# Optimization experiments

Hardware: AMD Instinct MI355X
Metric: run time of the kernel (lower is better)

Reference implementation:

```python
import jax, jax.numpy as jnp
import numpy as np

B, D = 16384, 512
EPS_COS = 1e-8  # torch cosine_similarity eps


def setup_inputs() -> dict:
    key = jax.random.key(0)
    ks = jax.random.split(key, 8)
    rep1 = jax.random.normal(ks[0], (B, D), jnp.float32)
    rep2 = jax.random.normal(ks[1], (B, D), jnp.float32)
    rep3 = jax.random.normal(ks[2], (B, D), jnp.float32)
    hazard = jax.random.normal(ks[3], (B, 1), jnp.float32)
    # F.nll_loss expects log-probabilities
    score = jax.nn.log_softmax(jax.random.normal(ks[4], (B, 2), jnp.float32), axis=-1)
    time = jax.random.uniform(ks[5], (B,), jnp.float32)
    event = jax.random.randint(ks[6], (B,), 0, 2, dtype=jnp.int32)
    perm = jax.random.permutation(ks[7], B)  # deterministic stand-in for shuffle()
    x1_idx = perm[: B // 2].astype(jnp.int32)
    x2_idx = perm[B // 2 :].astype(jnp.int32)
    return dict(rep1=rep1, rep2=rep2, rep3=rep3, hazard=hazard, score=score,
                time=time, event=event, x1_idx=x1_idx, x2_idx=x2_idx)


def _normalize(r):
    n = jnp.maximum(jnp.linalg.norm(r, axis=-1, keepdims=True), EPS_COS)
    return r / n


def reference(rep1, rep2, rep3, hazard, score, time, event, x1_idx, x2_idx):
    trade_off, margin, alpha, beta = 0.3, 0.2, 0.5, 0.5
    ev_f = event.astype(score.dtype)

    # ---- cross-entropy term: F.nll_loss(log_probs, event) ----
    nll = -jnp.mean(jnp.take_along_axis(score, event[:, None].astype(jnp.int32), axis=1))

    # ---- Cox negative log-likelihood ----
    order = jnp.argsort(-time)            # descending time
    risk = hazard[order, 0]               # [B]
    evs = ev_f[order]
    log_risk = jnp.log(jnp.cumsum(jnp.exp(risk)) + 1e-6)
    cox = -jnp.sum((risk - log_risk) * evs) / (jnp.sum(evs) + 1e-6)

    # ---- contrastive loss (3 modalities, vectorized over pairs) ----
    R = jnp.stack([_normalize(rep1), _normalize(rep2), _normalize(rep3)])  # [M,B,D]
    x = R[:, x1_idx]  # [M,P,D]
    y = R[:, x2_idx]  # [M,P,D]
    pairs = [(0, 1), (0, 2), (1, 2)]
    dis_xx = sum((x[i] * x[j]).sum(-1) for i, j in pairs)  # [P]
    dis_yy = sum((y[i] * y[j]).sum(-1) for i, j in pairs)  # [P]
    dis_xy = (x * y).sum(-1).sum(0)                         # [P]
    con = jnp.mean(jnp.log1p(jnp.exp(margin + dis_xy - alpha * dis_xx - beta * dis_yy)))

    return nll + cox + trade_off * con
```

## Files before the change

### kernel.cpp

```cpp
#include <hip/hip_runtime.h>
#include <math.h>

#define B_N     16384
#define D_N     512
#define NPAIR   8192
#define NBUCKET 16384
#define CON_BLOCKS 2048
#define STAT_BLOCKS 64
#define BIG_BLOCKS (CON_BLOCKS + STAT_BLOCKS)
#define COX_BLOCKS 64

__device__ __forceinline__ float wave_reduce(float v) {
    #pragma unroll
    for (int m = 32; m >= 1; m >>= 1) v += __shfl_xor(v, m, 64);
    return v;
}

__device__ __forceinline__ float dot4(float4 a, float4 b) {
    return a.x*b.x + a.y*b.y + a.z*b.z + a.w*b.w;
}

__device__ __forceinline__ int bucket_of(float t) {
    return min(max((int)(t * 16384.0f), 0), NBUCKET - 1);
}

__device__ __forceinline__ unsigned long long key_of(float t, int i) {
    return (((unsigned long long)__float_as_uint(t)) << 14) |
           (unsigned long long)(B_N - 1 - i);
}

__global__ __launch_bounds__(256) void k_big(
        const float* __restrict__ rep1,
        const float* __restrict__ rep2,
        const float* __restrict__ rep3,
        const float* __restrict__ hazard,
        const float* __restrict__ score,
        const float* __restrict__ time,
        const int*   __restrict__ event,
        const int*   __restrict__ x1_idx,
        const int*   __restrict__ x2_idx,
        float* __restrict__ partCon,
        float* __restrict__ partNll,
        float* __restrict__ partEv,
        float* __restrict__ sumE,
        int*   __restrict__ head,
        int*   __restrict__ next)
{
    __shared__ float sh0[4], sh1[4];
    const int tid  = threadIdx.x;
    const int lane = tid & 63;
    const int wave = tid >> 6;

    if (blockIdx.x < CON_BLOCKS) {
        const int p  = blockIdx.x * 4 + wave;
        const int ia = x1_idx[p];
        const int ib = x2_idx[p];
        const float4* A1 = (const float4*)(rep1 + (size_t)ia * D_N);
        const float4* A2 = (const float4*)(rep2 + (size_t)ia * D_N);
        const float4* A3 = (const float4*)(rep3 + (size_t)ia * D_N);
        const float4* B1 = (const float4*)(rep1 + (size_t)ib * D_N);
        const float4* B2 = (const float4*)(rep2 + (size_t)ib * D_N);
        const float4* B3 = (const float4*)(rep3 + (size_t)ib * D_N);

        float v[15];
        #pragma unroll
        for (int k = 0; k < 15; ++k) v[k] = 0.f;
        #pragma unroll
        for (int r = 0; r < 2; ++r) {
            const int k = lane + r * 64;
            float4 a1 = A1[k], a2 = A2[k], a3 = A3[k];
            float4 b1 = B1[k], b2 = B2[k], b3 = B3[k];
            v[0]  += dot4(a1, a1); v[1]  += dot4(a2, a2); v[2]  += dot4(a3, a3);
            v[3]  += dot4(b1, b1); v[4]  += dot4(b2, b2); v[5]  += dot4(b3, b3);
            v[6]  += dot4(a1, a2); v[7]  += dot4(a1, a3); v[8]  += dot4(a2, a3);
            v[9]  += dot4(b1, b2); v[10] += dot4(b1, b3); v[11] += dot4(b2, b3);
            v[12] += dot4(a1, b1); v[13] += dot4(a2, b2); v[14] += dot4(a3, b3);
        }
        #pragma unroll
        for (int k = 0; k < 15; ++k) v[k] = wave_reduce(v[k]);

        if (lane == 0) {
            float n1a = fmaxf(sqrtf(v[0]), 1e-8f), n2a = fmaxf(sqrtf(v[1]), 1e-8f), n3a = fmaxf(sqrtf(v[2]), 1e-8f);
            float n1b = fmaxf(sqrtf(v[3]), 1e-8f), n2b = fmaxf(sqrtf(v[4]), 1e-8f), n3b = fmaxf(sqrtf(v[5]), 1e-8f);
            float dxx = v[6]/(n1a*n2a) + v[7]/(n1a*n3a) + v[8]/(n2a*n3a);
            float dyy = v[9]/(n1b*n2b) + v[10]/(n1b*n3b) + v[11]/(n2b*n3b);
            float dxy = v[12]/(n1a*n1b) + v[13]/(n2a*n2b) + v[14]/(n3a*n3b);
            float s = 0.2f + dxy - 0.5f*dxx - 0.5f*dyy;
            sh0[wave] = log1pf(expf(s));
        }
        __syncthreads();
        if (tid == 0)
            partCon[blockIdx.x] = sh0[0] + sh0[1] + sh0[2] + sh0[3];
    } else {
        const int sb = blockIdx.x - CON_BLOCKS;
        const int i  = sb * 256 + tid;
        const float t = time[i];
        const float e = __expf(hazard[i]);
        const int   b = bucket_of(t);
        atomicAdd(&sumE[b], e);
        const int old = atomicExch(&head[b], i + 1);
        next[i] = old;

        const int ev = event[i];
        float nll_p = wave_reduce(score[i * 2 + ev]);
        float ev_p  = wave_reduce((float)ev);
        if (lane == 0) { sh0[wave] = nll_p; sh1[wave] = ev_p; }
        __syncthreads();
        if (tid == 0) {
            partNll[sb] = sh0[0] + sh0[1] + sh0[2] + sh0[3];
            partEv[sb]  = sh1[0] + sh1[1] + sh1[2] + sh1[3];
        }
    }
}

__global__ __launch_bounds__(1024) void k_scan(const float* __restrict__ sumE,
                                               float* __restrict__ cumH)
{
    __shared__ float lsf[1024];
    const int tid = threadIdx.x;
    const int base = tid * 16;

    float f[16]; float fs = 0.f;
    #pragma unroll
    for (int k = 0; k < 16; ++k) { f[k] = sumE[base + k]; fs += f[k]; }
    lsf[tid] = fs;
    __syncthreads();
    for (int d = 1; d < 1024; d <<= 1) {
        float v = (tid >= d) ? lsf[tid - d] : 0.f;
        __syncthreads();
        lsf[tid] += v;
        __syncthreads();
    }
    const float total = lsf[1023];
    float running = total - lsf[tid];
    #pragma unroll
    for (int k = 15; k >= 0; --k) { cumH[base + k] = running; running += f[k]; }
}

__global__ __launch_bounds__(256) void k_cox(
        const float* __restrict__ hazard,
        const float* __restrict__ time,
        const int*   __restrict__ event,
        const int*   __restrict__ head,
        const int*   __restrict__ next,
        const float* __restrict__ cumH,
        const float* __restrict__ partCon,
        const float* __restrict__ partNll,
        const float* __restrict__ partEv,
        float* __restrict__ partCox,
        int*   __restrict__ doneCox,
        float* __restrict__ out)
{
    __shared__ float shX[4];
    __shared__ int lastflag;
    const int tid  = threadIdx.x;
    const int lane = tid & 63;
    const int wave = tid >> 6;
    const int i = blockIdx.x * 256 + tid;

    const float t = time[i];
    const float h = hazard[i];
    const int   b = bucket_of(t);
    const unsigned long long ki = key_of(t, i);

    float cum = cumH[b] + __expf(h);
    int p = head[b];
    while (p) {
        const int j = p - 1;
        const float tj = time[j];
        if (key_of(tj, j) > ki) cum += __expf(hazard[j]);
        p = next[j];
    }
    float cox_p = event[i] ? (h - logf(cum + 1e-6f)) : 0.f;
    cox_p = wave_reduce(cox_p);
    if (lane == 0) shX[wave] = cox_p;
    __syncthreads();
    if (tid == 0)
        atomicExch(&partCox[blockIdx.x], shX[0] + shX[1] + shX[2] + shX[3]);

    __threadfence();
    if (tid == 0) lastflag = (atomicAdd(doneCox, 1) == COX_BLOCKS - 1);
    __syncthreads();
    if (lastflag) {
        float con = 0.f;
        #pragma unroll
        for (int k = 0; k < CON_BLOCKS / 256; ++k) con += partCon[tid + k * 256];
        float cox = 0.f, nll = 0.f, ev = 0.f;
        if (tid < COX_BLOCKS) {
            cox = atomicAdd(&partCox[tid], 0.f);
            nll = partNll[tid];
            ev  = partEv[tid];
        }
        con = wave_reduce(con);
        cox = wave_reduce(cox);
        nll = wave_reduce(nll);
        ev  = wave_reduce(ev);
        __syncthreads();
        if (lane == 0) { shX[wave] = con; }
        __syncthreads();
        float C = shX[0] + shX[1] + shX[2] + shX[3];
        if (lane == 0) { shX[wave] = cox; }
        __syncthreads();
        float X = shX[0] + shX[1] + shX[2] + shX[3];
        if (lane == 0) { shX[wave] = nll; }
        __syncthreads();
        float N = shX[0] + shX[1] + shX[2] + shX[3];
        if (lane == 0) { shX[wave] = ev; }
        __syncthreads();
        float E = shX[0] + shX[1] + shX[2] + shX[3];
        if (tid == 0)
            out[0] = (-N / (float)B_N) + (-X / (E + 1e-6f)) + 0.3f * (C / (float)NPAIR);
    }
}

extern "C" void kernel_launch(void* const* d_in, const int* in_sizes, int n_in,
                              void* d_out, int out_size, void* d_ws, size_t ws_size,
                              hipStream_t stream)
{
    const float* rep1   = (const float*)d_in[0];
    const float* rep2   = (const float*)d_in[1];
    const float* rep3   = (const float*)d_in[2];
    const float* hazard = (const float*)d_in[3];
    const float* score  = (const float*)d_in[4];
    const float* time_  = (const float*)d_in[5];
    const int*   event  = (const int*)d_in[6];
    const int*   x1     = (const int*)d_in[7];
    const int*   x2     = (const int*)d_in[8];
    float* out = (float*)d_out;

    char* w = (char*)d_ws;
    float* sumE    = (float*)(w + 0);
    int*   head    = (int*)  (w + 65536);
    int*   doneCox = (int*)  (w + 131072);
    int*   next    = (int*)  (w + 131136);
    float* cumH    = (float*)(w + 196672);
    float* partCon = (float*)(w + 262208);
    float* partNll = (float*)(w + 270400);
    float* partEv  = (float*)(w + 270656);
    float* partCox = (float*)(w + 270912);

    hipMemsetAsync(d_ws, 0, 131136, stream);

    k_big  <<<BIG_BLOCKS, 256, 0, stream>>>(rep1, rep2, rep3, hazard, score, time_,
                                            event, x1, x2, partCon, partNll, partEv,
                                            sumE, head, next);
    k_scan <<<1, 1024, 0, stream>>>(sumE, cumH);
    k_cox  <<<COX_BLOCKS, 256, 0, stream>>>(hazard, time_, event, head, next, cumH,
                                            partCon, partNll, partEv, partCox,
                                            doneCox, out);
}
```

Baseline: 150.8 us.

## Fuse bucket prefix-scan into stat blocks via last-block-done pattern

The separate single-block scan kernel is removed. The bucket prefix scan now runs inside the last-finishing stat block of the main kernel, found with an atomic completion counter. Stat blocks are moved to the front of the grid so they are scheduled first and their scan can overlap with the contrastive blocks. This saves one kernel launch and its dependency gap. The cost is a fence and atomic per stat block, plus a scan done by 256 threads instead of 1024.

```diff
diff --git a/kernel.cpp b/kernel.cpp
--- a/kernel.cpp
+++ b/kernel.cpp
@@ -5,9 +5,9 @@
 #define D_N     512
 #define NPAIR   8192
 #define NBUCKET 16384
+#define STAT_BLOCKS 64
 #define CON_BLOCKS 2048
-#define STAT_BLOCKS 64
-#define BIG_BLOCKS (CON_BLOCKS + STAT_BLOCKS)
+#define BIG_BLOCKS (STAT_BLOCKS + CON_BLOCKS)
 #define COX_BLOCKS 64
 
 __device__ __forceinline__ float wave_reduce(float v) {
@@ -44,15 +44,20 @@
         float* __restrict__ partEv,
         float* __restrict__ sumE,
         int*   __restrict__ head,
-        int*   __restrict__ next)
+        int*   __restrict__ next,
+        int*   __restrict__ doneStat,
+        float* __restrict__ cumH)
 {
     __shared__ float sh0[4], sh1[4];
+    __shared__ float lsf[256];
+    __shared__ int lastflag;
     const int tid  = threadIdx.x;
     const int lane = tid & 63;
     const int wave = tid >> 6;
 
-    if (blockIdx.x < CON_BLOCKS) {
-        const int p  = blockIdx.x * 4 + wave;
+    if (blockIdx.x >= STAT_BLOCKS) {
+        const int cb = blockIdx.x - STAT_BLOCKS;
+        const int p  = cb * 4 + wave;
         const int ia = x1_idx[p];
         const int ib = x2_idx[p];
         const float4* A1 = (const float4*)(rep1 + (size_t)ia * D_N);
@@ -90,51 +95,53 @@
         }
         __syncthreads();
         if (tid == 0)
-            partCon[blockIdx.x] = sh0[0] + sh0[1] + sh0[2] + sh0[3];
-    } else {
-        const int sb = blockIdx.x - CON_BLOCKS;
-        const int i  = sb * 256 + tid;
-        const float t = time[i];
-        const float e = __expf(hazard[i]);
-        const int   b = bucket_of(t);
-        atomicAdd(&sumE[b], e);
-        const int old = atomicExch(&head[b], i + 1);
-        next[i] = old;
-
-        const int ev = event[i];
-        float nll_p = wave_reduce(score[i * 2 + ev]);
-        float ev_p  = wave_reduce((float)ev);
-        if (lane == 0) { sh0[wave] = nll_p; sh1[wave] = ev_p; }
-        __syncthreads();
-        if (tid == 0) {
-            partNll[sb] = sh0[0] + sh0[1] + sh0[2] + sh0[3];
-            partEv[sb]  = sh1[0] + sh1[1] + sh1[2] + sh1[3];
-        }
-    }
-}
-
-__global__ __launch_bounds__(1024) void k_scan(const float* __restrict__ sumE,
-                                               float* __restrict__ cumH)
-{
-    __shared__ float lsf[1024];
-    const int tid = threadIdx.x;
-    const int base = tid * 16;
-
-    float f[16]; float fs = 0.f;
-    #pragma unroll
-    for (int k = 0; k < 16; ++k) { f[k] = sumE[base + k]; fs += f[k]; }
+            partCon[cb] = sh0[0] + sh0[1] + sh0[2] + sh0[3];
+        return;
+    }
+
+    const int sb = blockIdx.x;
+    const int i  = sb * 256 + tid;
+    const float t = time[i];
+    const float e = __expf(hazard[i]);
+    const int   b = bucket_of(t);
+    atomicAdd(&sumE[b], e);
+    const int old = atomicExch(&head[b], i + 1);
+    next[i] = old;
+
+    const int ev = event[i];
+    float nll_p = wave_reduce(score[i * 2 + ev]);
+    float ev_p  = wave_reduce((float)ev);
+    if (lane == 0) { sh0[wave] = nll_p; sh1[wave] = ev_p; }
+    __syncthreads();
+    if (tid == 0) {
+        partNll[sb] = sh0[0] + sh0[1] + sh0[2] + sh0[3];
+        partEv[sb]  = sh1[0] + sh1[1] + sh1[2] + sh1[3];
+    }
+
+    __threadfence();
+    __syncthreads();
+    if (tid == 0) lastflag = (atomicAdd(doneStat, 1) == STAT_BLOCKS - 1);
+    __syncthreads();
+    if (!lastflag) return;
+
+    volatile float* vs = sumE;
+    const int base = tid * (NBUCKET / 256);
+    float fs = 0.f;
+    for (int k = 0; k < NBUCKET / 256; ++k) fs += vs[base + k];
     lsf[tid] = fs;
     __syncthreads();
-    for (int d = 1; d < 1024; d <<= 1) {
+    for (int d = 1; d < 256; d <<= 1) {
         float v = (tid >= d) ? lsf[tid - d] : 0.f;
         __syncthreads();
         lsf[tid] += v;
         __syncthreads();
     }
-    const float total = lsf[1023];
-    float running = total - lsf[tid];
-    #pragma unroll
-    for (int k = 15; k >= 0; --k) { cumH[base + k] = running; running += f[k]; }
+    const float total = lsf[255];
+    float run = total - lsf[tid];
+    for (int k = NBUCKET / 256 - 1; k >= 0; --k) {
+        cumH[base + k] = run;
+        run += vs[base + k];
+    }
 }
 
 __global__ __launch_bounds__(256) void k_cox(
@@ -229,23 +236,23 @@
     float* out = (float*)d_out;
 
     char* w = (char*)d_ws;
-    float* sumE    = (float*)(w + 0);
-    int*   head    = (int*)  (w + 65536);
-    int*   doneCox = (int*)  (w + 131072);
-    int*   next    = (int*)  (w + 131136);
-    float* cumH    = (float*)(w + 196672);
-    float* partCon = (float*)(w + 262208);
-    float* partNll = (float*)(w + 270400);
-    float* partEv  = (float*)(w + 270656);
-    float* partCox = (float*)(w + 270912);
+    float* sumE     = (float*)(w + 0);
+    int*   head     = (int*)  (w + 65536);
+    int*   doneStat = (int*)  (w + 131072);
+    int*   doneCox  = (int*)  (w + 131076);
+    int*   next     = (int*)  (w + 131136);
+    float* cumH     = (float*)(w + 196672);
+    float* partCon  = (float*)(w + 262208);
+    float* partNll  = (float*)(w + 270400);
+    float* partEv   = (float*)(w + 270656);
+    float* partCox  = (float*)(w + 270912);
 
     hipMemsetAsync(d_ws, 0, 131136, stream);
 
-    k_big  <<<BIG_BLOCKS, 256, 0, stream>>>(rep1, rep2, rep3, hazard, score, time_,
-                                            event, x1, x2, partCon, partNll, partEv,
-                                            sumE, head, next);
-    k_scan <<<1, 1024, 0, stream>>>(sumE, cumH);
-    k_cox  <<<COX_BLOCKS, 256, 0, stream>>>(hazard, time_, event, head, next, cumH,
-                                            partCon, partNll, partEv, partCox,
-                                            doneCox, out);
-}
+    k_big <<<BIG_BLOCKS, 256, 0, stream>>>(rep1, rep2, rep3, hazard, score, time_,
+                                           event, x1, x2, partCon, partNll, partEv,
+                                           sumE, head, next, doneStat, cumH);
+    k_cox <<<COX_BLOCKS, 256, 0, stream>>>(hazard, time_, event, head, next, cumH,
+                                           partCon, partNll, partEv, partCox,
+                                           doneCox, out);
+}
```

New measurement: 174.0 us. 15.4% more time.
